# Kernel tuning notes

Measured on AMD Instinct MI355X. Metric: run time of the kernel, lower is better.

## Reference

```python
import jax, jax.numpy as jnp
import numpy as np

EPS = 1e-5


def conv1x1(x, w):
    # x: (N, C, V, T), w: (O, C) -> (N, O, V, T)
    return jnp.einsum('ncvt,oc->novt', x, w)


def batchnorm2d(y, gamma, beta):
    # training-mode BN over (N, V, T) per channel, biased variance (torch semantics)
    mean = jnp.mean(y, axis=(0, 2, 3), keepdims=True)
    var = jnp.mean((y - mean) ** 2, axis=(0, 2, 3), keepdims=True)
    yhat = (y - mean) * jax.lax.rsqrt(var + EPS)
    return yhat * gamma[None, :, None, None] + beta[None, :, None, None]


def spatial_g(x, wg1, wg2):
    # learned adjacency: softmax over last dim of (N, T, V, V)
    a1 = conv1x1(x, wg1)  # (N, O, V, T)
    a2 = conv1x1(x, wg2)  # (N, O, V, T)
    g = jnp.einsum('novt,nout->ntvu', a1, a2)  # (N, T, V, V)
    return jax.nn.softmax(g, axis=-1)


def gcn_unit(x, g, w1, w2, gamma, beta):
    # message passing: g (N,T,V,V) applied over joint dim of x (N,C,V,T)
    x1 = jnp.einsum('ntvu,ncut->ncvt', g, x)
    y = conv1x1(x1, w1) + conv1x1(x, w2)
    return jax.nn.relu(batchnorm2d(y, gamma, beta))


def setup_inputs() -> dict:
    key = jax.random.key(0)
    ks = jax.random.split(key, 12)
    N, C, V, T = 64, 64, 25, 128
    dims = [64, 64, 128, 256]
    gp = 16
    s = 0.05
    inp = {
        'x': jax.random.normal(ks[0], (N, C, V, T), jnp.float32),
        'wg1': jax.random.normal(ks[1], (gp, dims[0]), jnp.float32) * s,
        'wg2': jax.random.normal(ks[2], (gp, dims[0]), jnp.float32) * s,
        'w11': jax.random.normal(ks[3], (dims[1], dims[0]), jnp.float32) * s,
        'w12': jax.random.normal(ks[4], (dims[1], dims[0]), jnp.float32) * s,
        'gamma1': jnp.ones((dims[1],), jnp.float32),
        'beta1': jnp.zeros((dims[1],), jnp.float32),
        'w21': jax.random.normal(ks[5], (dims[2], dims[1]), jnp.float32) * s,
        'w22': jax.random.normal(ks[6], (dims[2], dims[1]), jnp.float32) * s,
        'gamma2': jnp.ones((dims[2],), jnp.float32),
        'beta2': jnp.zeros((dims[2],), jnp.float32),
        'w31': jax.random.normal(ks[7], (dims[3], dims[2]), jnp.float32) * s,
        'w32': jax.random.normal(ks[8], (dims[3], dims[2]), jnp.float32) * s,
        'gamma3': jnp.ones((dims[3],), jnp.float32),
        'beta3': jnp.zeros((dims[3],), jnp.float32),
    }
    return inp


def reference(x, wg1, wg2, w11, w12, gamma1, beta1, w21, w22, gamma2, beta2,
              w31, w32, gamma3, beta3):
    g = spatial_g(x, wg1, wg2)                       # shared adjacency (N,T,V,V)
    x = gcn_unit(x, g, w11, w12, gamma1, beta1)      # (N, 64, V, T)
    x = gcn_unit(x, g, w21, w22, gamma2, beta2)      # (N, 128, V, T)
    x = gcn_unit(x, g, w31, w32, gamma3, beta3)      # (N, 256, V, T)
    return x, g
```

## Files before the change

kernel.cpp:

```cpp
#include <hip/hip_runtime.h>
#include <cstdint>

#define V_ 25
#define T_ 128
#define VT_ 3200
#define NVTF_ 204800.0f

typedef unsigned short ushort_t;
typedef __attribute__((ext_vector_type(8))) short s16x8;
typedef __attribute__((ext_vector_type(4))) float f32x4;

#define SW(r, ch) ((ch) ^ ((r) & 7) ^ (((r) >> 3) & 7))

__device__ __forceinline__ ushort_t f2bf(float f) {
    union { float f; unsigned u; } v; v.f = f;
    unsigned r = v.u + 0x7FFFu + ((v.u >> 16) & 1u);
    return (ushort_t)(r >> 16);
}
__device__ __forceinline__ float bf2f(ushort_t h) {
    union { unsigned u; float f; } v; v.u = ((unsigned)h) << 16;
    return v.f;
}
__device__ __forceinline__ unsigned cvtpk(float lo, float hi) {
    unsigned r;
    asm volatile("v_cvt_pk_bf16_f32 %0, %1, %2" : "=v"(r) : "v"(lo), "v"(hi));
    return r;
}
__device__ __forceinline__ void gload16(const void* g, void* l) {
    __builtin_amdgcn_global_load_lds((const __attribute__((address_space(1))) void*)g,
                                     (__attribute__((address_space(3))) void*)l, 16, 0, 0);
}

__global__ __launch_bounds__(128) void k_a(const float* __restrict__ x,
        const float* __restrict__ wg1, const float* __restrict__ wg2,
        ushort_t* __restrict__ a1, ushort_t* __restrict__ a2,
        ushort_t* __restrict__ xb,
        const float* __restrict__ w11, const float* __restrict__ w12,
        const float* __restrict__ w21, const float* __restrict__ w22,
        const float* __restrict__ w31, const float* __restrict__ w32,
        ushort_t* __restrict__ Wc) {
    int b = blockIdx.x; int n = b / V_; int v = b % V_;
    int t = threadIdx.x;
    int wi = b * 128 + t;
    if (wi < 90112) {
        float wv;
        if (wi < 8192) {
            int o = wi >> 7, k = wi & 127;
            wv = (k < 64) ? w11[o * 64 + k] : w12[o * 64 + k - 64];
        } else if (wi < 24576) {
            int j = wi - 8192; int o = j >> 7, k = j & 127;
            wv = (k < 64) ? w21[o * 64 + k] : w22[o * 64 + k - 64];
        } else {
            int j = wi - 24576; int o = j >> 8, k = j & 255;
            wv = (k < 128) ? w31[o * 128 + k] : w32[o * 128 + k - 128];
        }
        Wc[wi] = f2bf(wv);
    }
    __shared__ float w1s[1024], w2s[1024];
    for (int i = threadIdx.x; i < 1024; i += 128) { w1s[i] = wg1[i]; w2s[i] = wg2[i]; }
    __syncthreads();
    float s1[16], s2[16];
    #pragma unroll
    for (int o = 0; o < 16; o++) { s1[o] = 0.f; s2[o] = 0.f; }
    s16x8 xs[8];
    const float* xp = x + (size_t)n * 204800 + v * T_ + t;
    #pragma unroll
    for (int c = 0; c < 64; c++) {
        float xv = xp[(size_t)c * VT_];
        xs[c >> 3][c & 7] = (short)f2bf(xv);
        #pragma unroll
        for (int o = 0; o < 16; o++) {
            s1[o] = fmaf(w1s[o*64+c], xv, s1[o]);
            s2[o] = fmaf(w2s[o*64+c], xv, s2[o]);
        }
    }
    size_t abase = (size_t)n * 51200 + v * T_ + t;
    #pragma unroll
    for (int o = 0; o < 16; o++) {
        a1[abase + (size_t)o * VT_] = f2bf(s1[o]);
        a2[abase + (size_t)o * VT_] = f2bf(s2[o]);
    }
    ushort_t* cp = xb + (size_t)(n * VT_ + v * T_ + t) * 64;
    #pragma unroll
    for (int ch = 0; ch < 8; ch++) *(s16x8*)(cp + ch * 8) = xs[ch];
}

__global__ __launch_bounds__(256) void k_g(const ushort_t* __restrict__ a1,
        const ushort_t* __restrict__ a2, float* __restrict__ g,
        ushort_t* __restrict__ gb) {
    int n = blockIdx.x >> 3; int t0 = (blockIdx.x & 7) * 16;
    __shared__ float A1s[6400], A2s[6400];
    for (int i = threadIdx.x; i < 6400; i += 256) {
        int o = i / 400; int r = i % 400; int v = r >> 4; int tt = r & 15;
        size_t ga = (size_t)n * 51200 + (size_t)o * VT_ + v * T_ + t0 + tt;
        A1s[i] = bf2f(a1[ga]);
        A2s[i] = bf2f(a2[ga]);
    }
    __syncthreads();
    for (int r = threadIdx.x; r < 400; r += 256) {
        int v = r >> 4; int tt = r & 15;
        float a1r[16];
        #pragma unroll
        for (int o = 0; o < 16; o++) a1r[o] = A1s[o*400 + v*16 + tt];
        float gr[25];
        float mx = -1e30f;
        for (int u = 0; u < 25; u++) {
            float s = 0.f;
            #pragma unroll
            for (int o = 0; o < 16; o++) s = fmaf(a1r[o], A2s[o*400 + u*16 + tt], s);
            gr[u] = s; mx = fmaxf(mx, s);
        }
        float sum = 0.f;
        for (int u = 0; u < 25; u++) { gr[u] = __expf(gr[u] - mx); sum += gr[u]; }
        float inv = 1.f / sum;
        float* gp = g + ((size_t)(n * T_ + t0 + tt) * V_ + v) * V_;
        ushort_t* gbp = gb + ((size_t)((n * 128 + t0 + tt) * 25 + v)) * 32;
        for (int u = 0; u < 25; u++) {
            float val = gr[u] * inv;
            gp[u] = val;
            gbp[u] = f2bf(val);
        }
        #pragma unroll
        for (int u = 25; u < 32; u++) gbp[u] = 0;
    }
}

template<int C, bool BNB, bool XBSRC, int TOUT, int OPASS>
__global__ __launch_bounds__(256) void k_fgemm(
        const ushort_t* __restrict__ Wc, const ushort_t* __restrict__ ysrc,
        const ushort_t* __restrict__ gb,
        const float* __restrict__ bns, const float* __restrict__ bnb,
        ushort_t* __restrict__ yt,
        float* __restrict__ psum, float* __restrict__ psq) {
    constexpr int K2 = 2 * C;
    constexpr int KSTEPS = K2 / 32;
    constexpr int NC8 = C / 8;
    constexpr int NCT = C / 16;
    constexpr int HKS = C / 32;
    constexpr int MROWS = 100;
    constexpr int MI = 7;
    constexpr int XBYTES = (TOUT == 0) ? 14400 : 16;
    __shared__ __align__(16) ushort_t YS[MROWS * C];
    __shared__ __align__(16) ushort_t MPo[MROWS * C];
    __shared__ __align__(16) char XTRA[XBYTES];
    ushort_t* Lw = (ushort_t*)XTRA;

    int n = blockIdx.y, mb = blockIdx.x;
    int m0 = mb * MROWS, tb = mb * 4;
    int tid = threadIdx.x, w = tid >> 6, lane = tid & 63;
    int l15 = lane & 15, g4 = lane >> 4;

    for (int i = tid; i < MROWS * NC8; i += 256) {
        int yr = i / NC8, cc = i % NC8;
        size_t saddr;
        if (XBSRC) {
            int t = tb + yr / 25, v = yr % 25;
            saddr = (size_t)n * 204800 + (size_t)(v * 128 + t) * 64 + cc * 8;
        } else {
            saddr = ((size_t)n * VT_ + m0 + yr) * C + cc * 8;
        }
        s16x8 vv = *(const s16x8*)(ysrc + saddr);
        if (BNB) {
            int ob = cc * 8;
            float4 s0 = *(const float4*)(bns + ob), s1 = *(const float4*)(bns + ob + 4);
            float4 h0 = *(const float4*)(bnb + ob), h1 = *(const float4*)(bnb + ob + 4);
            float sc[8] = {s0.x, s0.y, s0.z, s0.w, s1.x, s1.y, s1.z, s1.w};
            float sh[8] = {h0.x, h0.y, h0.z, h0.w, h1.x, h1.y, h1.z, h1.w};
            float ff[8];
            #pragma unroll
            for (int j = 0; j < 8; j++)
                ff[j] = fmaxf(fmaf(bf2f((ushort_t)vv[j]), sc[j], sh[j]), 0.f);
            union { unsigned u[4]; s16x8 s; } U;
            U.u[0] = cvtpk(ff[0], ff[1]); U.u[1] = cvtpk(ff[2], ff[3]);
            U.u[2] = cvtpk(ff[4], ff[5]); U.u[3] = cvtpk(ff[6], ff[7]);
            vv = U.s;
        }
        *(s16x8*)(YS + ((size_t)yr * NC8 + SW(yr, cc)) * 8) = vv;
    }
    __syncthreads();
    {
        int tl = w;
        const ushort_t* gbase = gb + ((size_t)((n * 128 + tb + tl) * 25)) * 32;
        s16x8 aG0 = *(const s16x8*)(gbase + (size_t)(l15) * 32 + g4 * 8);
        s16x8 aG1 = *(const s16x8*)(gbase + (size_t)(16 + l15) * 32 + g4 * 8);
        #pragma unroll
        for (int ct = 0; ct < NCT; ct++) {
            int c = ct * 16 + l15;
            int cc = c >> 3, sub = c & 7;
            s16x8 bF;
            #pragma unroll
            for (int j = 0; j < 8; j++) {
                int u = g4 * 8 + j;
                int uu = (u > 24) ? 24 : u;
                int r = tl * 25 + uu;
                bF[j] = (short)YS[((size_t)r * NC8 + SW(r, cc)) * 8 + sub];
            }
            f32x4 z = {};
            f32x4 d0 = __builtin_amdgcn_mfma_f32_16x16x32_bf16(aG0, bF, z, 0, 0, 0);
            f32x4 d1 = __builtin_amdgcn_mfma_f32_16x16x32_bf16(aG1, bF, z, 0, 0, 0);
            #pragma unroll
            for (int b = 0; b < 4; b++) {
                int v0 = g4 * 4 + b;
                int r0 = tl * 25 + v0;
                MPo[((size_t)r0 * NC8 + SW(r0, cc)) * 8 + sub] = f2bf(d0[b]);
                int v1 = 16 + g4 * 4 + b;
                if (v1 < 25) {
                    int r1 = tl * 25 + v1;
                    MPo[((size_t)r1 * NC8 + SW(r1, cc)) * 8 + sub] = f2bf(d1[b]);
                }
            }
        }
    }
    __syncthreads();
    for (int pass = 0; pass < OPASS; pass++) {
        int o0 = pass * 64;
        s16x8 aReg[KSTEPS];
        const ushort_t* ap = Wc + (size_t)(o0 + w * 16 + l15) * K2 + g4 * 8;
        #pragma unroll
        for (int ks = 0; ks < KSTEPS; ks++)
            aReg[ks] = *(const s16x8*)(ap + ks * 32);
        f32x4 acc[MI] = {};
        __builtin_amdgcn_s_setprio(1);
        #pragma unroll
        for (int ks = 0; ks < KSTEPS; ks++) {
            const ushort_t* bbase = (ks < HKS) ? MPo : YS;
            int ksl = (ks < HKS) ? ks : ks - HKS;
            #pragma unroll
            for (int mi = 0; mi < MI; mi++) {
                int r = mi * 16 + l15;
                int rr = (r < MROWS) ? r : (MROWS - 1);
                int ch = ksl * 4 + g4;
                s16x8 bF = *(const s16x8*)(bbase + ((size_t)rr * NC8 + SW(rr, ch)) * 8);
                acc[mi] = __builtin_amdgcn_mfma_f32_16x16x32_bf16(aReg[ks], bF, acc[mi], 0, 0, 0);
            }
        }
        __builtin_amdgcn_s_setprio(0);
        int p = n * 32 + mb;
        #pragma unroll
        for (int b = 0; b < 4; b++) {
            float ss = 0.f, qq = 0.f;
            #pragma unroll
            for (int mi = 0; mi < MI; mi++) {
                float v0 = acc[mi][b];
                if (mi == 6 && l15 >= 4) v0 = 0.f;
                ss += v0; qq = fmaf(v0, v0, qq);
            }
            #pragma unroll
            for (int msk = 1; msk < 16; msk <<= 1) {
                ss += __shfl_xor(ss, msk, 16);
                qq += __shfl_xor(qq, msk, 16);
            }
            if (l15 == 0) {
                int o = o0 + w * 16 + g4 * 4 + b;
                psum[(size_t)o * 2048 + p] = ss;
                psq [(size_t)o * 2048 + p] = qq;
            }
        }
        if (TOUT == 0) {
            __syncthreads();
            #pragma unroll
            for (int mi = 0; mi < MI; mi++) {
                int r = mi * 16 + l15;
                if (r < MROWS) {
                    unsigned lo = cvtpk(acc[mi][0], acc[mi][1]);
                    unsigned hi = cvtpk(acc[mi][2], acc[mi][3]);
                    *(unsigned*)(Lw + r * 72 + w * 16 + g4 * 4)     = lo;
                    *(unsigned*)(Lw + r * 72 + w * 16 + g4 * 4 + 2) = hi;
                }
            }
            __syncthreads();
            for (int i = tid; i < MROWS * 8; i += 256) {
                int r = i >> 3, oc = i & 7;
                s16x8 pk = *(const s16x8*)(Lw + r * 72 + oc * 8);
                *(s16x8*)(yt + ((size_t)n * VT_ + m0 + r) * (OPASS * 64) + o0 + oc * 8) = pk;
            }
        } else {
            int obase = n * 256 + o0 + w * 16 + g4 * 4;
            #pragma unroll
            for (int mi = 0; mi < MI; mi++) {
                int r = mi * 16 + l15;
                if (r < MROWS) {
                    #pragma unroll
                    for (int b = 0; b < 4; b++)
                        yt[(size_t)(obase + b) * VT_ + m0 + r] = f2bf(acc[mi][b]);
                }
            }
        }
    }
}

__global__ __launch_bounds__(256) void k_stats(const float* __restrict__ psum,
        const float* __restrict__ psq, const float* __restrict__ gamma,
        const float* __restrict__ beta, float* __restrict__ bns,
        float* __restrict__ bnb) {
    int o = blockIdx.x;
    float s = 0.f, q = 0.f;
    for (int i = threadIdx.x; i < 2048; i += 256) {
        s += psum[(size_t)o*2048+i]; q += psq[(size_t)o*2048+i];
    }
    __shared__ float rs[256], rq[256];
    rs[threadIdx.x] = s; rq[threadIdx.x] = q;
    __syncthreads();
    for (int st = 128; st > 0; st >>= 1) {
        if (threadIdx.x < st) { rs[threadIdx.x] += rs[threadIdx.x+st]; rq[threadIdx.x] += rq[threadIdx.x+st]; }
        __syncthreads();
    }
    if (threadIdx.x == 0) {
        float mean = rs[0] / NVTF_;
        float var = rq[0] / NVTF_ - mean * mean;
        float scale = gamma[o] * rsqrtf(var + 1e-5f);
        bns[o] = scale;
        bnb[o] = beta[o] - mean * scale;
    }
}

__global__ __launch_bounds__(256) void k_bnf(const ushort_t* __restrict__ y3,
        const float* __restrict__ bns, const float* __restrict__ bnb,
        float* __restrict__ xout) {
    __shared__ __align__(16) ushort_t L[8 * VT_];
    int n = blockIdx.y, oc = blockIdx.x;
    size_t base = (size_t)(n * 256 + oc * 8) * VT_;
    for (int i = threadIdx.x; i < 3200; i += 256)
        gload16(y3 + base + (size_t)i * 8, (char*)L + i * 16);
    __syncthreads();
    for (int i = threadIdx.x; i < 6400; i += 256) {
        int t4 = i & 31, v = (i >> 5) % 25, o = i / 800;
        int og = oc * 8 + o;
        float sc = bns[og], sh = bnb[og];
        int lb = o * VT_ + v;
        float4 f;
        f.x = fmaxf(fmaf(bf2f(L[lb + (t4*4+0)*25]), sc, sh), 0.f);
        f.y = fmaxf(fmaf(bf2f(L[lb + (t4*4+1)*25]), sc, sh), 0.f);
        f.z = fmaxf(fmaf(bf2f(L[lb + (t4*4+2)*25]), sc, sh), 0.f);
        f.w = fmaxf(fmaf(bf2f(L[lb + (t4*4+3)*25]), sc, sh), 0.f);
        *(float4*)(xout + (size_t)(n * 256 + og) * VT_ + v * T_ + t4 * 4) = f;
    }
}

extern "C" void kernel_launch(void* const* d_in, const int* in_sizes, int n_in,
                              void* d_out, int out_size, void* d_ws, size_t ws_size,
                              hipStream_t stream) {
    const float* x   = (const float*)d_in[0];
    const float* wg1 = (const float*)d_in[1];
    const float* wg2 = (const float*)d_in[2];
    const float* w11 = (const float*)d_in[3];
    const float* w12 = (const float*)d_in[4];
    const float* ga1 = (const float*)d_in[5];
    const float* be1 = (const float*)d_in[6];
    const float* w21 = (const float*)d_in[7];
    const float* w22 = (const float*)d_in[8];
    const float* ga2 = (const float*)d_in[9];
    const float* be2 = (const float*)d_in[10];
    const float* w31 = (const float*)d_in[11];
    const float* w32 = (const float*)d_in[12];
    const float* ga3 = (const float*)d_in[13];
    const float* be3 = (const float*)d_in[14];

    float* xout = (float*)d_out;
    float* gout = xout + 52428800;

    float* ws = (float*)d_ws;
    ushort_t* xb  = (ushort_t*)(ws + 0);
    ushort_t* a1  = (ushort_t*)(ws + 6553600);
    ushort_t* a2  = (ushort_t*)(ws + 8192000);
    ushort_t* y1  = (ushort_t*)(ws + 9830400);
    ushort_t* y2  = (ushort_t*)(ws + 16384000);
    ushort_t* y3  = (ushort_t*)(ws + 29491200);
    ushort_t* gb  = (ushort_t*)(ws + 55705600);
    float* psum = ws + 58982400;
    float* psq  = ws + 59506688;
    ushort_t* Wc = (ushort_t*)(ws + 60030976);
    float* bns  = ws + 60076032;
    float* bnb  = ws + 60076288;
    ushort_t* Wc1 = Wc, *Wc2 = Wc + 8192, *Wc3 = Wc + 24576;

    k_a<<<1600, 128, 0, stream>>>(x, wg1, wg2, a1, a2, xb,
                                  w11, w12, w21, w22, w31, w32, Wc);
    k_g<<<512, 256, 0, stream>>>(a1, a2, gout, gb);

    k_fgemm<64, false, true, 0, 1><<<dim3(32, 64), 256, 0, stream>>>(
        Wc1, xb, gb, nullptr, nullptr, y1, psum, psq);
    k_stats<<<64, 256, 0, stream>>>(psum, psq, ga1, be1, bns, bnb);

    k_fgemm<64, true, false, 0, 2><<<dim3(32, 64), 256, 0, stream>>>(
        Wc2, y1, gb, bns, bnb, y2, psum, psq);
    k_stats<<<128, 256, 0, stream>>>(psum, psq, ga2, be2, bns, bnb);

    k_fgemm<128, true, false, 2, 4><<<dim3(32, 64), 256, 0, stream>>>(
        Wc3, y2, gb, bns, bnb, y3, psum, psq);
    k_stats<<<256, 256, 0, stream>>>(psum, psq, ga3, be3, bns, bnb);

    k_bnf<<<dim3(32, 64), 256, 0, stream>>>(y3, bns, bnb, xout);
}
```

Before: 292.1 us.

## Replace BN stats kernels with atomic accumulation and in-kernel scale computation

Per-block BatchNorm partial sums are now accumulated with atomicAdd into a small per-channel buffer, zeroed in the first kernel. Each consumer GEMM and the final BN kernel compute scale and shift into shared memory themselves. This removes three separate stats reduction launches and their global partial-sum arrays. In exchange, summation order becomes nondeterministic and the per-block scale computation is redundant.

```diff
diff --git a/kernel.cpp b/kernel.cpp
--- a/kernel.cpp
+++ b/kernel.cpp
@@ -38,9 +38,12 @@
         const float* __restrict__ w11, const float* __restrict__ w12,
         const float* __restrict__ w21, const float* __restrict__ w22,
         const float* __restrict__ w31, const float* __restrict__ w32,
-        ushort_t* __restrict__ Wc) {
+        ushort_t* __restrict__ Wc, float* __restrict__ PS) {
     int b = blockIdx.x; int n = b / V_; int v = b % V_;
     int t = threadIdx.x;
+    if (b == 0) {
+        for (int i = t; i < 896; i += 128) PS[i] = 0.f;
+    }
     int wi = b * 128 + t;
     if (wi < 90112) {
         float wv;
@@ -129,9 +132,10 @@
 __global__ __launch_bounds__(256) void k_fgemm(
         const ushort_t* __restrict__ Wc, const ushort_t* __restrict__ ysrc,
         const ushort_t* __restrict__ gb,
-        const float* __restrict__ bns, const float* __restrict__ bnb,
-        ushort_t* __restrict__ yt,
-        float* __restrict__ psum, float* __restrict__ psq) {
+        const float* __restrict__ gin, const float* __restrict__ bin,
+        const float* __restrict__ psI, const float* __restrict__ pqI,
+        float* __restrict__ psO, float* __restrict__ pqO,
+        ushort_t* __restrict__ yt) {
     constexpr int K2 = 2 * C;
     constexpr int KSTEPS = K2 / 32;
     constexpr int NC8 = C / 8;
@@ -139,17 +143,29 @@
     constexpr int HKS = C / 32;
     constexpr int MROWS = 100;
     constexpr int MI = 7;
-    constexpr int XBYTES = (TOUT == 0) ? 14400 : 16;
+    constexpr int XBYTES = (TOUT == 0) ? 14400 : 1024;
     __shared__ __align__(16) ushort_t YS[MROWS * C];
     __shared__ __align__(16) ushort_t MPo[MROWS * C];
     __shared__ __align__(16) char XTRA[XBYTES];
     ushort_t* Lw = (ushort_t*)XTRA;
+    float* bnsS = (float*)XTRA;
+    float* bnbS = (float*)(XTRA + 512);
 
     int n = blockIdx.y, mb = blockIdx.x;
     int m0 = mb * MROWS, tb = mb * 4;
     int tid = threadIdx.x, w = tid >> 6, lane = tid & 63;
     int l15 = lane & 15, g4 = lane >> 4;
 
+    if (BNB) {
+        for (int i = tid; i < C; i += 256) {
+            float mean = psI[i] * (1.0f / NVTF_);
+            float var  = pqI[i] * (1.0f / NVTF_) - mean * mean;
+            float sc = gin[i] * rsqrtf(var + 1e-5f);
+            bnsS[i] = sc;
+            bnbS[i] = bin[i] - mean * sc;
+        }
+        __syncthreads();
+    }
     for (int i = tid; i < MROWS * NC8; i += 256) {
         int yr = i / NC8, cc = i % NC8;
         size_t saddr;
@@ -162,8 +178,8 @@
         s16x8 vv = *(const s16x8*)(ysrc + saddr);
         if (BNB) {
             int ob = cc * 8;
-            float4 s0 = *(const float4*)(bns + ob), s1 = *(const float4*)(bns + ob + 4);
-            float4 h0 = *(const float4*)(bnb + ob), h1 = *(const float4*)(bnb + ob + 4);
+            float4 s0 = *(const float4*)(bnsS + ob), s1 = *(const float4*)(bnsS + ob + 4);
+            float4 h0 = *(const float4*)(bnbS + ob), h1 = *(const float4*)(bnbS + ob + 4);
             float sc[8] = {s0.x, s0.y, s0.z, s0.w, s1.x, s1.y, s1.z, s1.w};
             float sh[8] = {h0.x, h0.y, h0.z, h0.w, h1.x, h1.y, h1.z, h1.w};
             float ff[8];
@@ -235,7 +251,6 @@
             }
         }
         __builtin_amdgcn_s_setprio(0);
-        int p = n * 32 + mb;
         #pragma unroll
         for (int b = 0; b < 4; b++) {
             float ss = 0.f, qq = 0.f;
@@ -252,8 +267,8 @@
             }
             if (l15 == 0) {
                 int o = o0 + w * 16 + g4 * 4 + b;
-                psum[(size_t)o * 2048 + p] = ss;
-                psq [(size_t)o * 2048 + p] = qq;
+                atomicAdd(&psO[o], ss);
+                atomicAdd(&pqO[o], qq);
             }
         }
         if (TOUT == 0) {
@@ -289,36 +304,21 @@
     }
 }
 
-__global__ __launch_bounds__(256) void k_stats(const float* __restrict__ psum,
-        const float* __restrict__ psq, const float* __restrict__ gamma,
-        const float* __restrict__ beta, float* __restrict__ bns,
-        float* __restrict__ bnb) {
-    int o = blockIdx.x;
-    float s = 0.f, q = 0.f;
-    for (int i = threadIdx.x; i < 2048; i += 256) {
-        s += psum[(size_t)o*2048+i]; q += psq[(size_t)o*2048+i];
-    }
-    __shared__ float rs[256], rq[256];
-    rs[threadIdx.x] = s; rq[threadIdx.x] = q;
-    __syncthreads();
-    for (int st = 128; st > 0; st >>= 1) {
-        if (threadIdx.x < st) { rs[threadIdx.x] += rs[threadIdx.x+st]; rq[threadIdx.x] += rq[threadIdx.x+st]; }
-        __syncthreads();
-    }
-    if (threadIdx.x == 0) {
-        float mean = rs[0] / NVTF_;
-        float var = rq[0] / NVTF_ - mean * mean;
-        float scale = gamma[o] * rsqrtf(var + 1e-5f);
-        bns[o] = scale;
-        bnb[o] = beta[o] - mean * scale;
-    }
-}
-
 __global__ __launch_bounds__(256) void k_bnf(const ushort_t* __restrict__ y3,
-        const float* __restrict__ bns, const float* __restrict__ bnb,
+        const float* __restrict__ gin, const float* __restrict__ bin,
+        const float* __restrict__ psI, const float* __restrict__ pqI,
         float* __restrict__ xout) {
     __shared__ __align__(16) ushort_t L[8 * VT_];
+    __shared__ float bnsS[256], bnbS[256];
     int n = blockIdx.y, oc = blockIdx.x;
+    {
+        int i = threadIdx.x;
+        float mean = psI[i] * (1.0f / NVTF_);
+        float var  = pqI[i] * (1.0f / NVTF_) - mean * mean;
+        float sc = gin[i] * rsqrtf(var + 1e-5f);
+        bnsS[i] = sc;
+        bnbS[i] = bin[i] - mean * sc;
+    }
     size_t base = (size_t)(n * 256 + oc * 8) * VT_;
     for (int i = threadIdx.x; i < 3200; i += 256)
         gload16(y3 + base + (size_t)i * 8, (char*)L + i * 16);
@@ -326,7 +326,7 @@
     for (int i = threadIdx.x; i < 6400; i += 256) {
         int t4 = i & 31, v = (i >> 5) % 25, o = i / 800;
         int og = oc * 8 + o;
-        float sc = bns[og], sh = bnb[og];
+        float sc = bnsS[og], sh = bnbS[og];
         int lb = o * VT_ + v;
         float4 f;
         f.x = fmaxf(fmaf(bf2f(L[lb + (t4*4+0)*25]), sc, sh), 0.f);
@@ -367,28 +367,25 @@
     ushort_t* y2  = (ushort_t*)(ws + 16384000);
     ushort_t* y3  = (ushort_t*)(ws + 29491200);
     ushort_t* gb  = (ushort_t*)(ws + 55705600);
-    float* psum = ws + 58982400;
-    float* psq  = ws + 59506688;
-    ushort_t* Wc = (ushort_t*)(ws + 60030976);
-    float* bns  = ws + 60076032;
-    float* bnb  = ws + 60076288;
+    float* PS   = ws + 58982400;
+    ushort_t* Wc = (ushort_t*)(ws + 58983424);
+    float* ps1 = PS,        *pq1 = PS + 64;
+    float* ps2 = PS + 128,  *pq2 = PS + 256;
+    float* ps3 = PS + 384,  *pq3 = PS + 640;
     ushort_t* Wc1 = Wc, *Wc2 = Wc + 8192, *Wc3 = Wc + 24576;
 
     k_a<<<1600, 128, 0, stream>>>(x, wg1, wg2, a1, a2, xb,
-                                  w11, w12, w21, w22, w31, w32, Wc);
+                                  w11, w12, w21, w22, w31, w32, Wc, PS);
     k_g<<<512, 256, 0, stream>>>(a1, a2, gout, gb);
 
     k_fgemm<64, false, true, 0, 1><<<dim3(32, 64), 256, 0, stream>>>(
-        Wc1, xb, gb, nullptr, nullptr, y1, psum, psq);
-    k_stats<<<64, 256, 0, stream>>>(psum, psq, ga1, be1, bns, bnb);
+        Wc1, xb, gb, nullptr, nullptr, nullptr, nullptr, ps1, pq1, y1);
 
     k_fgemm<64, true, false, 0, 2><<<dim3(32, 64), 256, 0, stream>>>(
-        Wc2, y1, gb, bns, bnb, y2, psum, psq);
-    k_stats<<<128, 256, 0, stream>>>(psum, psq, ga2, be2, bns, bnb);
+        Wc2, y1, gb, ga1, be1, ps1, pq1, ps2, pq2, y2);
 
     k_fgemm<128, true, false, 2, 4><<<dim3(32, 64), 256, 0, stream>>>(
-        Wc3, y2, gb, bns, bnb, y3, psum, psq);
-    k_stats<<<256, 256, 0, stream>>>(psum, psq, ga3, be3, bns, bnb);
-
-    k_bnf<<<dim3(32, 64), 256, 0, stream>>>(y3, bns, bnb, xout);
-}
+        Wc3, y2, gb, ga2, be2, ps2, pq2, ps3, pq3, y3);
+
+    k_bnf<<<dim3(32, 64), 256, 0, stream>>>(y3, ga3, be3, ps3, pq3, xout);
+}
```

Measured after the change: 863.3 us. +195.5%, slower.
